# Kernel optimization log

Measured on AMD Instinct MI355X. Metric: run time of the kernel, lower is better.

## Reference

```python
import jax, jax.numpy as jnp
from jax import lax
import numpy as np

DIM = 48
HEADS = 2
HIDDEN = 96  # int(dim * 2.0)
EPS_LN = 1e-5
EPS_NORM = 1e-12


def _ln(x, w, b):
    # WithBias LayerNorm over channel dim (dim=1 in NCHW == last dim in b,(hw),c)
    mu = jnp.mean(x, axis=1, keepdims=True)
    var = jnp.var(x, axis=1, keepdims=True)
    return (x - mu) / jnp.sqrt(var + EPS_LN) * w[None, :, None, None] + b[None, :, None, None]


def _conv1x1(x, w, b):
    # w: [O, C, 1, 1]
    return jnp.einsum('bchw,oc->bohw', x, w[:, :, 0, 0]) + b[None, :, None, None]


def _dwconv3(x, w, b):
    # w: [C, 1, 3, 3], groups=C
    y = lax.conv_general_dilated(x, w, (1, 1), 'SAME',
                                 feature_group_count=x.shape[1],
                                 dimension_numbers=('NCHW', 'OIHW', 'NCHW'))
    return y + b[None, :, None, None]


def _l2norm(x):
    n = jnp.sqrt(jnp.sum(x * x, axis=-1, keepdims=True))
    return x / jnp.maximum(n, EPS_NORM)


def setup_inputs() -> dict:
    key = jax.random.key(0)
    ks = jax.random.split(key, 12)
    s = 0.02
    inp = {
        'x': jax.random.normal(ks[0], (2, DIM, 64, 64), jnp.float32),
        'norm1_w': jnp.ones((DIM,), jnp.float32),
        'norm1_b': jnp.zeros((DIM,), jnp.float32),
        'qkv_w': jax.random.normal(ks[1], (DIM * 3, DIM, 1, 1), jnp.float32) * s,
        'qkv_b': jnp.zeros((DIM * 3,), jnp.float32),
        'qkvdw_w': jax.random.normal(ks[2], (DIM * 3, 1, 3, 3), jnp.float32) * s,
        'qkvdw_b': jnp.zeros((DIM * 3,), jnp.float32),
        'temperature': jnp.ones((HEADS, 1, 1), jnp.float32),
        'proj_w': jax.random.normal(ks[3], (DIM, DIM, 1, 1), jnp.float32) * s,
        'proj_b': jnp.zeros((DIM,), jnp.float32),
        'norm2_w': jnp.ones((DIM,), jnp.float32),
        'norm2_b': jnp.zeros((DIM,), jnp.float32),
        'fi_w': jax.random.normal(ks[4], (HIDDEN * 2, DIM, 1, 1), jnp.float32) * s,
        'fi_b': jnp.zeros((HIDDEN * 2,), jnp.float32),
        'fdw_w': jax.random.normal(ks[5], (HIDDEN * 2, 1, 3, 3), jnp.float32) * s,
        'fdw_b': jnp.zeros((HIDDEN * 2,), jnp.float32),
        'fo_w': jax.random.normal(ks[6], (DIM, HIDDEN, 1, 1), jnp.float32) * s,
        'fo_b': jnp.zeros((DIM,), jnp.float32),
    }
    return inp


def _block(x, norm1_w, norm1_b, qkv_w, qkv_b, qkvdw_w, qkvdw_b, temperature,
           proj_w, proj_b, norm2_w, norm2_b, fi_w, fi_b, fdw_w, fdw_b, fo_w, fo_b):
    b, c, h, w = x.shape
    n = h * w
    chead = c // HEADS
    # --- attention branch ---
    xn = _ln(x, norm1_w, norm1_b)
    qkv = _dwconv3(_conv1x1(xn, qkv_w, qkv_b), qkvdw_w, qkvdw_b)
    q, k, v = jnp.split(qkv, 3, axis=1)
    def to_heads(t):  # [b, heads*chead, h, w] -> [b, heads, n, chead]
        return t.reshape(b, HEADS, chead, n).transpose(0, 1, 3, 2)
    q, k, v = to_heads(q), to_heads(k), to_heads(v)
    q = _l2norm(q)
    k = _l2norm(k)
    attn = jnp.einsum('bhnc,bhmc->bhnm', q, k) * temperature[None]
    attn = jax.nn.softmax(attn, axis=-1)
    out = jnp.einsum('bhnm,bhmc->bhnc', attn, v)
    out = out.transpose(0, 1, 3, 2).reshape(b, c, h, w)
    x = x + _conv1x1(out, proj_w, proj_b)
    # --- ffn branch ---
    xn = _ln(x, norm2_w, norm2_b)
    y = _dwconv3(_conv1x1(xn, fi_w, fi_b), fdw_w, fdw_b)
    y1, y2 = jnp.split(y, 2, axis=1)
    y = jax.nn.gelu(y1, approximate=False) * y2
    x = x + _conv1x1(y, fo_w, fo_b)
    return x


def reference(x, norm1_w, norm1_b, qkv_w, qkv_b, qkvdw_w, qkvdw_b, temperature,
              proj_w, proj_b, norm2_w, norm2_b, fi_w, fi_b, fdw_w, fdw_b, fo_w, fo_b):
    return _block(x, norm1_w, norm1_b, qkv_w, qkv_b, qkvdw_w, qkvdw_b, temperature,
                  proj_w, proj_b, norm2_w, norm2_b, fi_w, fi_b, fdw_w, fdw_b, fo_w, fo_b)
```

## Files before the change

### kernel.cpp

```cpp
#include <hip/hip_runtime.h>
#include <hip/hip_bf16.h>
#include <math.h>

#define NPIX 4096
#define NB 2

typedef __attribute__((ext_vector_type(8))) short short8;
typedef __attribute__((ext_vector_type(4))) short short4s;
typedef __attribute__((ext_vector_type(4))) float floatx4;

static __device__ inline short f2bf(float f) {
    union { float f; unsigned u; } v; v.f = f;
    unsigned r = (v.u + 0x7FFFu + ((v.u >> 16) & 1u)) >> 16;
    return (short)r;
}
static __device__ inline float bf2f(short s) {
    union { unsigned u; float f; } v;
    v.u = ((unsigned)(unsigned short)s) << 16;
    return v.f;
}
static __device__ inline unsigned pk2(float a, float b) {
    __hip_bfloat162 pk = __float22bfloat162_rn(make_float2(a, b));
    return *(unsigned*)&pk;
}

__global__ void k_prepw(const float* __restrict__ qkvw, const float* __restrict__ fiw,
                        const float* __restrict__ fow, const float* __restrict__ projw,
                        short* __restrict__ qkvwbf, short* __restrict__ fiwbf,
                        short* __restrict__ fowbf, short* __restrict__ projwbf) {
    int idx = blockIdx.x * 256 + threadIdx.x;
    if (idx < 144 * 64) {
        int o = idx >> 6, c = idx & 63;
        qkvwbf[idx] = (c < 48) ? f2bf(qkvw[o * 48 + c]) : (short)0;
        return;
    }
    idx -= 144 * 64;
    if (idx < 192 * 64) {
        int o = idx >> 6, c = idx & 63;
        fiwbf[idx] = (c < 48) ? f2bf(fiw[o * 48 + c]) : (short)0;
        return;
    }
    idx -= 192 * 64;
    if (idx < 48 * 96) {
        fowbf[idx] = f2bf(fow[idx]);
        return;
    }
    idx -= 48 * 96;
    if (idx < 48 * 64) {
        int o = idx >> 6, c = idx & 63;
        int h = c >> 5, cc = c & 31;
        projwbf[idx] = (cc < 24) ? f2bf(projw[o * 48 + h * 24 + cc]) : (short)0;
    }
}

__global__ __launch_bounds__(256) void k_qkv_fused(
    const float* __restrict__ xin, const float* __restrict__ n1w, const float* __restrict__ n1b,
    const short* __restrict__ qkvwbf, const float* __restrict__ qkvb,
    const float* __restrict__ dww, const float* __restrict__ dwb,
    const float* __restrict__ temp,
    short* __restrict__ Qbf, short* __restrict__ Kbf, short* __restrict__ Vbf)
{
    int px0 = blockIdx.x * 16;
    int y = blockIdx.y, b = blockIdx.z;
    int t = threadIdx.x;
    int w = t >> 6, lane = t & 63, l15 = lane & 15, quad = lane >> 4;

    __shared__ __align__(16) short xn[64][72];
    __shared__ short qkv[64][148];
    __shared__ float q2[16][148];
    __shared__ float red[4][64], redq[4][64];
    __shared__ float muS[64], rsS[64];
    __shared__ float dwwS[1296], dwbS[144];
    __shared__ short vmask[64];

    for (int u = t; u < 1296; u += 256) dwwS[u] = dww[u];
    if (t < 144) dwbS[t] = dwb[t];

    int pp = t & 63, cg = t >> 6;
    int rr = pp / 18, ix = pp - rr * 18;
    int yy = y + rr - 1, xpx = px0 - 1 + ix;
    bool pv = (pp < 54) && ((unsigned)yy < 64u) && ((unsigned)xpx < 64u);
    if (cg == 0) vmask[pp] = pv ? (short)1 : (short)0;

    float v[12]; float s = 0.f, sq = 0.f;
    if (pv) {
        size_t pbase = (size_t)(yy * 64 + xpx);
#pragma unroll
        for (int j = 0; j < 12; j++) {
            float vv = xin[((size_t)b * 48 + cg * 12 + j) * NPIX + pbase];
            v[j] = vv; s += vv; sq += vv * vv;
        }
    } else {
#pragma unroll
        for (int j = 0; j < 12; j++) v[j] = 0.f;
    }
    red[cg][pp] = s; redq[cg][pp] = sq;
    __syncthreads();
    if (t < 64) {
        float ss = red[0][t] + red[1][t] + red[2][t] + red[3][t];
        float qq = redq[0][t] + redq[1][t] + redq[2][t] + redq[3][t];
        float mu = ss * (1.f / 48.f);
        float var = qq * (1.f / 48.f) - mu * mu;
        muS[t] = mu; rsS[t] = rsqrtf(var + 1e-5f);
    }
    __syncthreads();
    {
        float mu = muS[pp], rs = rsS[pp];
#pragma unroll
        for (int j = 0; j < 12; j++) {
            int c = cg * 12 + j;
            xn[pp][c] = f2bf((v[j] - mu) * rs * n1w[c] + n1b[c]);
        }
        short8 z8 = {};
        if (cg == 0) *(short8*)&xn[pp][48] = z8;
        else if (cg == 1) *(short8*)&xn[pp][56] = z8;
    }
    __syncthreads();
    floatx4 zf = {0.f, 0.f, 0.f, 0.f};
    for (int job = w; job < 36; job += 4) {
        int pt = job / 9, ot = job % 9;
        short8 a0 = *(const short8*)&xn[pt * 16 + l15][quad * 8];
        short8 a1 = *(const short8*)&xn[pt * 16 + l15][32 + quad * 8];
        const short* wb = qkvwbf + (ot * 16 + l15) * 64;
        short8 b0 = *(const short8*)(wb + quad * 8);
        short8 b1 = *(const short8*)(wb + 32 + quad * 8);
        floatx4 c = __builtin_amdgcn_mfma_f32_16x16x32_bf16(a0, b0, zf, 0, 0, 0);
        c = __builtin_amdgcn_mfma_f32_16x16x32_bf16(a1, b1, c, 0, 0, 0);
        int oc = ot * 16 + l15;
        float bi = qkvb[oc];
#pragma unroll
        for (int r = 0; r < 4; r++) {
            int opp = pt * 16 + quad * 4 + r;
            qkv[opp][oc] = vmask[opp] ? f2bf(c[r] + bi) : (short)0;
        }
    }
    __syncthreads();
    {
        int i = t & 15, g = t >> 4;
        for (int cc = 0; cc < 9; cc++) {
            int c = g * 9 + cc;
            const float* wp = dwwS + c * 9;
            float acc = dwbS[c];
#pragma unroll
            for (int dy = 0; dy < 3; dy++)
#pragma unroll
                for (int dx = 0; dx < 3; dx++)
                    acc += bf2f(qkv[dy * 18 + i + dx][c]) * wp[dy * 3 + dx];
            q2[i][c] = acc;
        }
    }
    __syncthreads();
    if (t < 128) {
        int i = t & 15, h = (t >> 4) & 1, sel = t >> 5;
        int n = y * 64 + px0 + i;
        int bh = b * 2 + h;
        if (sel < 2) {
            float vv2[24]; float ss = 0.f;
            int base = sel * 48 + h * 24;
#pragma unroll
            for (int c = 0; c < 24; c++) { vv2[c] = q2[i][base + c]; ss += vv2[c] * vv2[c]; }
            float sc = ((sel == 0) ? temp[h] : 1.f) / fmaxf(sqrtf(ss), 1e-12f);
            short qs[32];
#pragma unroll
            for (int c = 0; c < 24; c++) qs[c] = f2bf(vv2[c] * sc);
#pragma unroll
            for (int c = 24; c < 32; c++) qs[c] = 0;
            short* dst = ((sel == 0) ? Qbf : Kbf) + ((size_t)bh * NPIX + n) * 32;
#pragma unroll
            for (int i8 = 0; i8 < 4; i8++) {
                short8 st;
#pragma unroll
                for (int j = 0; j < 8; j++) st[j] = qs[i8 * 8 + j];
                *(short8*)(dst + i8 * 8) = st;
            }
        } else {
            int half = sel - 2;
            int r5 = n & 31;
            int pos = (r5 < 16) ? ((r5 >> 2) * 8 + (r5 & 3))
                                : (((r5 & 15) >> 2) * 8 + (r5 & 3) + 4);
            int vcol = (n & ~31) + pos;
#pragma unroll
            for (int cc = 0; cc < 12; cc++) {
                int c = half * 12 + cc;
                Vbf[((size_t)bh * 32 + c) * NPIX + vcol] = f2bf(q2[i][96 + h * 24 + c]);
            }
            if (half == 1) {
#pragma unroll
                for (int c = 24; c < 32; c++)
                    Vbf[((size_t)bh * 32 + c) * NPIX + vcol] = 0;
            }
        }
    }
}

__global__ __launch_bounds__(1024) void k_attn_mfma2(
    const short* __restrict__ Qbf, const short* __restrict__ Kbf,
    const short* __restrict__ Vbf, short* __restrict__ O)
{
    int qt = blockIdx.x, bh = blockIdx.y;
    int t = threadIdx.x;
    int tg = t & 255, g = t >> 8;
    int wloc = (t >> 6) & 3, lane = t & 63, l15 = lane & 15, quad = lane >> 4;

    __shared__ __align__(16) short tileK[4][2][64][40];
    __shared__ __align__(16) short tileV[4][2][32][72];
    __shared__ float Ocomb[4][64][33];
    __shared__ float Lcomb[4][64];

    int qrow0 = qt * 64 + wloc * 16;
    short8 bq = *(const short8*)(Qbf + ((size_t)bh * NPIX + qrow0 + l15) * 32 + quad * 8);

    int krow = tg >> 2, kseg = tg & 3;
    int vch = tg >> 3, vseg = tg & 7;
    const short* srcK = Kbf + ((size_t)bh * NPIX + krow) * 32 + kseg * 8;
    const short* srcV = Vbf + ((size_t)(bh * 32 + vch)) * NPIX + vseg * 8;

    int key0 = g * 1024;
    *(short8*)&tileK[g][0][krow][kseg * 8] = *(const short8*)(srcK + (size_t)key0 * 32);
    *(short8*)&tileV[g][0][vch][vseg * 8]  = *(const short8*)(srcV + key0);

    floatx4 zf = {0.f, 0.f, 0.f, 0.f};
    floatx4 o0 = zf, o1 = zf;
    float ls = 0.f;

    const int NKT = 16;
    for (int kt = 0; kt < NKT; kt++) {
        __syncthreads();
        int cur = kt & 1;
        short8 ldK = {}, ldV = {};
        if (kt < NKT - 1) {
            int kabs = key0 + (kt + 1) * 64;
            ldK = *(const short8*)(srcK + (size_t)kabs * 32);
            ldV = *(const short8*)(srcV + kabs);
        }
        short8 ka0 = *(const short8*)&tileK[g][cur][l15][quad * 8];
        short8 ka1 = *(const short8*)&tileK[g][cur][16 + l15][quad * 8];
        short8 ka2 = *(const short8*)&tileK[g][cur][32 + l15][quad * 8];
        short8 ka3 = *(const short8*)&tileK[g][cur][48 + l15][quad * 8];
        floatx4 s0 = __builtin_amdgcn_mfma_f32_16x16x32_bf16(ka0, bq, zf, 0, 0, 0);
        floatx4 s1 = __builtin_amdgcn_mfma_f32_16x16x32_bf16(ka1, bq, zf, 0, 0, 0);
        floatx4 s2 = __builtin_amdgcn_mfma_f32_16x16x32_bf16(ka2, bq, zf, 0, 0, 0);
        floatx4 s3 = __builtin_amdgcn_mfma_f32_16x16x32_bf16(ka3, bq, zf, 0, 0, 0);
        float e0[4], e1[4], e2[4], e3[4];
#pragma unroll
        for (int r = 0; r < 4; r++) {
            e0[r] = __expf(s0[r]); e1[r] = __expf(s1[r]);
            e2[r] = __expf(s2[r]); e3[r] = __expf(s3[r]);
            ls += (e0[r] + e1[r]) + (e2[r] + e3[r]);
        }
        short8 p01, p23;
        {
            unsigned* u01 = (unsigned*)&p01;
            unsigned* u23 = (unsigned*)&p23;
            u01[0] = pk2(e0[0], e0[1]); u01[1] = pk2(e0[2], e0[3]);
            u01[2] = pk2(e1[0], e1[1]); u01[3] = pk2(e1[2], e1[3]);
            u23[0] = pk2(e2[0], e2[1]); u23[1] = pk2(e2[2], e2[3]);
            u23[2] = pk2(e3[0], e3[1]); u23[3] = pk2(e3[2], e3[3]);
        }
        short8 va00 = *(const short8*)&tileV[g][cur][l15][quad * 8];
        short8 va01 = *(const short8*)&tileV[g][cur][l15][32 + quad * 8];
        short8 va10 = *(const short8*)&tileV[g][cur][16 + l15][quad * 8];
        short8 va11 = *(const short8*)&tileV[g][cur][16 + l15][32 + quad * 8];
        o0 = __builtin_amdgcn_mfma_f32_16x16x32_bf16(va00, p01, o0, 0, 0, 0);
        o0 = __builtin_amdgcn_mfma_f32_16x16x32_bf16(va01, p23, o0, 0, 0, 0);
        o1 = __builtin_amdgcn_mfma_f32_16x16x32_bf16(va10, p01, o1, 0, 0, 0);
        o1 = __builtin_amdgcn_mfma_f32_16x16x32_bf16(va11, p23, o1, 0, 0, 0);
        if (kt < NKT - 1) {
            *(short8*)&tileK[g][1 - cur][krow][kseg * 8] = ldK;
            *(short8*)&tileV[g][1 - cur][vch][vseg * 8]  = ldV;
        }
    }
    ls += __shfl_xor(ls, 16, 64);
    ls += __shfl_xor(ls, 32, 64);
    int qi = wloc * 16 + l15;
#pragma unroll
    for (int r = 0; r < 4; r++) {
        Ocomb[g][qi][quad * 4 + r]      = o0[r];
        Ocomb[g][qi][16 + quad * 4 + r] = o1[r];
    }
    if (quad == 0) Lcomb[g][qi] = ls;
    __syncthreads();
    {
        int qq = t >> 4, cp = t & 15;
        float l4 = Lcomb[0][qq] + Lcomb[1][qq] + Lcomb[2][qq] + Lcomb[3][qq];
        float inv = 1.f / l4;
        float sa = (Ocomb[0][qq][2 * cp] + Ocomb[1][qq][2 * cp] +
                    Ocomb[2][qq][2 * cp] + Ocomb[3][qq][2 * cp]) * inv;
        float sb = (Ocomb[0][qq][2 * cp + 1] + Ocomb[1][qq][2 * cp + 1] +
                    Ocomb[2][qq][2 * cp + 1] + Ocomb[3][qq][2 * cp + 1]) * inv;
        int b = bh >> 1, h = bh & 1;
        int n = qt * 64 + qq;
        *(unsigned*)(O + ((size_t)b * NPIX + n) * 64 + h * 32 + 2 * cp) = pk2(sa, sb);
    }
}

__global__ __launch_bounds__(256) void k_tail_fused(
    const float* __restrict__ xin, const short* __restrict__ O,
    const short* __restrict__ projwbf, const float* __restrict__ projb,
    const float* __restrict__ n2w, const float* __restrict__ n2b,
    const short* __restrict__ fiwbf, const float* __restrict__ fib,
    const float* __restrict__ fdww, const float* __restrict__ fdwb,
    const short* __restrict__ fowbf, const float* __restrict__ fob,
    float* __restrict__ out)
{
    int px0 = blockIdx.x * 16;
    int y = blockIdx.y, b = blockIdx.z;
    int t = threadIdx.x;
    int w = t >> 6, lane = t & 63, l15 = lane & 15, quad = lane >> 4;

    __shared__ float x1s[64][53];
    __shared__ __align__(16) short xn2[64][72];
    __shared__ short ypre[56][196];
    __shared__ __align__(16) short yv[16][104];
    __shared__ float red[4][64], redq[4][64];
    __shared__ float muS[64], rsS[64];
    __shared__ float fdwwS[1728], fdwbS[192];
    __shared__ short vmask[64];
    __shared__ int nidx[64];

    for (int u = t; u < 1728; u += 256) fdwwS[u] = fdww[u];
    if (t < 192) fdwbS[t] = fdwb[t];
    if (t < 64) {
        int rr = t / 18, ix = t - rr * 18;
        int yy = y + rr - 1, xpx = px0 - 1 + ix;
        bool pv = (t < 54) && ((unsigned)yy < 64u) && ((unsigned)xpx < 64u);
        vmask[t] = pv ? (short)1 : (short)0;
        int n = yy * 64 + xpx;
        n = n < 0 ? 0 : (n > 4095 ? 4095 : n);
        nidx[t] = n;
    }
    __syncthreads();

    floatx4 zf = {0.f, 0.f, 0.f, 0.f};
    for (int job = w; job < 12; job += 4) {
        int pt = job / 3, ot = job % 3;
        const short* oa = O + ((size_t)b * NPIX + nidx[pt * 16 + l15]) * 64;
        short8 a0 = *(const short8*)(oa + quad * 8);
        short8 a1 = *(const short8*)(oa + 32 + quad * 8);
        const short* wb = projwbf + (ot * 16 + l15) * 64;
        short8 b0 = *(const short8*)(wb + quad * 8);
        short8 b1 = *(const short8*)(wb + 32 + quad * 8);
        floatx4 c = __builtin_amdgcn_mfma_f32_16x16x32_bf16(a0, b0, zf, 0, 0, 0);
        c = __builtin_amdgcn_mfma_f32_16x16x32_bf16(a1, b1, c, 0, 0, 0);
        int oc = ot * 16 + l15;
        float bi = projb[oc];
#pragma unroll
        for (int r = 0; r < 4; r++) {
            int opp = pt * 16 + quad * 4 + r;
            x1s[opp][oc] = xin[((size_t)b * 48 + oc) * NPIX + nidx[opp]] + c[r] + bi;
        }
    }
    __syncthreads();
    int pp = t & 63, cg = t >> 6;
    {
        float v[12]; float s = 0.f, sq = 0.f;
#pragma unroll
        for (int j = 0; j < 12; j++) {
            float vv = x1s[pp][cg * 12 + j];
            v[j] = vv; s += vv; sq += vv * vv;
        }
        red[cg][pp] = s; redq[cg][pp] = sq;
        __syncthreads();
        if (t < 64) {
            float ss = red[0][t] + red[1][t] + red[2][t] + red[3][t];
            float qq = redq[0][t] + redq[1][t] + redq[2][t] + redq[3][t];
            float mu = ss * (1.f / 48.f);
            float var = qq * (1.f / 48.f) - mu * mu;
            muS[t] = mu; rsS[t] = rsqrtf(var + 1e-5f);
        }
        __syncthreads();
        float mu = muS[pp], rs = rsS[pp];
#pragma unroll
        for (int j = 0; j < 12; j++) {
            int c = cg * 12 + j;
            xn2[pp][c] = f2bf((v[j] - mu) * rs * n2w[c] + n2b[c]);
        }
        short8 z8 = {};
        if (cg == 0) *(short8*)&xn2[pp][48] = z8;
        else if (cg == 1) *(short8*)&xn2[pp][56] = z8;
    }
    __syncthreads();
    for (int job = w; job < 48; job += 4) {
        int pt = job / 12, ot = job % 12;
        short8 a0 = *(const short8*)&xn2[pt * 16 + l15][quad * 8];
        short8 a1 = *(const short8*)&xn2[pt * 16 + l15][32 + quad * 8];
        const short* wb = fiwbf + (ot * 16 + l15) * 64;
        short8 b0 = *(const short8*)(wb + quad * 8);
        short8 b1 = *(const short8*)(wb + 32 + quad * 8);
        floatx4 c = __builtin_amdgcn_mfma_f32_16x16x32_bf16(a0, b0, zf, 0, 0, 0);
        c = __builtin_amdgcn_mfma_f32_16x16x32_bf16(a1, b1, c, 0, 0, 0);
        int oc = ot * 16 + l15;
        float bi = fib[oc];
#pragma unroll
        for (int r = 0; r < 4; r++) {
            int opp = pt * 16 + quad * 4 + r;
            if (opp < 56) ypre[opp][oc] = vmask[opp] ? f2bf(c[r] + bi) : (short)0;
        }
    }
    __syncthreads();
    {
        int i = t & 15, gg = t >> 4;
        for (int cc = 0; cc < 6; cc++) {
            int c = gg * 6 + cc;
            const float* wp  = fdwwS + c * 9;
            const float* wp2 = fdwwS + (c + 96) * 9;
            float a = fdwbS[c], g2v = fdwbS[c + 96];
#pragma unroll
            for (int dy = 0; dy < 3; dy++)
#pragma unroll
                for (int dx = 0; dx < 3; dx++) {
                    int ppi = dy * 18 + i + dx;
                    a   += bf2f(ypre[ppi][c])      * wp[dy * 3 + dx];
                    g2v += bf2f(ypre[ppi][c + 96]) * wp2[dy * 3 + dx];
                }
            float ge = 0.5f * a * (1.f + erff(a * 0.70710678118654752f));
            yv[i][c] = f2bf(ge * g2v);
        }
        short8 z8 = {};
        if (gg == 0) *(short8*)&yv[i][96] = z8;
    }
    __syncthreads();
    if (w < 3) {
        floatx4 c = zf;
#pragma unroll
        for (int k = 0; k < 3; k++) {
            short8 a  = *(const short8*)&yv[l15][k * 32 + quad * 8];
            short8 bb = *(const short8*)(fowbf + (w * 16 + l15) * 96 + k * 32 + quad * 8);
            c = __builtin_amdgcn_mfma_f32_16x16x32_bf16(a, bb, c, 0, 0, 0);
        }
        int oc = w * 16 + l15;
        float bi = fob[oc];
#pragma unroll
        for (int r = 0; r < 4; r++) {
            int i = quad * 4 + r;
            size_t idx = ((size_t)b * 48 + oc) * NPIX + y * 64 + px0 + i;
            out[idx] = x1s[19 + i][oc] + c[r] + bi;
        }
    }
}

extern "C" void kernel_launch(void* const* d_in, const int* in_sizes, int n_in,
                              void* d_out, int out_size, void* d_ws, size_t ws_size,
                              hipStream_t stream) {
    const float* x       = (const float*)d_in[0];
    const float* n1w     = (const float*)d_in[1];
    const float* n1b     = (const float*)d_in[2];
    const float* qkv_w   = (const float*)d_in[3];
    const float* qkv_b   = (const float*)d_in[4];
    const float* qkvdw_w = (const float*)d_in[5];
    const float* qkvdw_b = (const float*)d_in[6];
    const float* temp    = (const float*)d_in[7];
    const float* proj_w  = (const float*)d_in[8];
    const float* proj_b  = (const float*)d_in[9];
    const float* n2w     = (const float*)d_in[10];
    const float* n2b     = (const float*)d_in[11];
    const float* fi_w    = (const float*)d_in[12];
    const float* fi_b    = (const float*)d_in[13];
    const float* fdw_w   = (const float*)d_in[14];
    const float* fdw_b   = (const float*)d_in[15];
    const float* fo_w    = (const float*)d_in[16];
    const float* fo_b    = (const float*)d_in[17];

    short* sws = (short*)d_ws;
    short* Qbf     = sws;
    short* Kbf     = Qbf + 524288;
    short* Vbf     = Kbf + 524288;
    short* Obuf    = Vbf + 524288;
    short* qkvwbf  = Obuf + 524288;
    short* fiwbf   = qkvwbf + 9216;
    short* fowbf   = fiwbf + 12288;
    short* projwbf = fowbf + 4608;

    {
        int total = 144 * 64 + 192 * 64 + 48 * 96 + 48 * 64;
        k_prepw<<<(total + 255) / 256, 256, 0, stream>>>(qkv_w, fi_w, fo_w, proj_w,
                                                         qkvwbf, fiwbf, fowbf, projwbf);
    }
    {
        dim3 g(4, 64, NB);
        k_qkv_fused<<<g, 256, 0, stream>>>(x, n1w, n1b, qkvwbf, qkv_b,
                                           qkvdw_w, qkvdw_b, temp, Qbf, Kbf, Vbf);
    }
    {
        dim3 g(64, 4);
        k_attn_mfma2<<<g, 1024, 0, stream>>>(Qbf, Kbf, Vbf, Obuf);
    }
    {
        dim3 g(4, 64, NB);
        k_tail_fused<<<g, 256, 0, stream>>>(x, Obuf, projwbf, proj_b, n2w, n2b,
                                            fiwbf, fi_b, fdw_w, fdw_b, fowbf, fo_b,
                                            (float*)d_out);
    }
}
```

Baseline: 139.5 us.

## Fold weight bf16 conversion into qkv kernel and switch softmax to exp2

```diff
diff --git a/kernel.cpp b/kernel.cpp
--- a/kernel.cpp
+++ b/kernel.cpp
@@ -6,7 +6,6 @@
 #define NB 2
 
 typedef __attribute__((ext_vector_type(8))) short short8;
-typedef __attribute__((ext_vector_type(4))) short short4s;
 typedef __attribute__((ext_vector_type(4))) float floatx4;
 
 static __device__ inline short f2bf(float f) {
@@ -24,41 +23,15 @@
     return *(unsigned*)&pk;
 }
 
-__global__ void k_prepw(const float* __restrict__ qkvw, const float* __restrict__ fiw,
-                        const float* __restrict__ fow, const float* __restrict__ projw,
-                        short* __restrict__ qkvwbf, short* __restrict__ fiwbf,
-                        short* __restrict__ fowbf, short* __restrict__ projwbf) {
-    int idx = blockIdx.x * 256 + threadIdx.x;
-    if (idx < 144 * 64) {
-        int o = idx >> 6, c = idx & 63;
-        qkvwbf[idx] = (c < 48) ? f2bf(qkvw[o * 48 + c]) : (short)0;
-        return;
-    }
-    idx -= 144 * 64;
-    if (idx < 192 * 64) {
-        int o = idx >> 6, c = idx & 63;
-        fiwbf[idx] = (c < 48) ? f2bf(fiw[o * 48 + c]) : (short)0;
-        return;
-    }
-    idx -= 192 * 64;
-    if (idx < 48 * 96) {
-        fowbf[idx] = f2bf(fow[idx]);
-        return;
-    }
-    idx -= 48 * 96;
-    if (idx < 48 * 64) {
-        int o = idx >> 6, c = idx & 63;
-        int h = c >> 5, cc = c & 31;
-        projwbf[idx] = (cc < 24) ? f2bf(projw[o * 48 + h * 24 + cc]) : (short)0;
-    }
-}
-
 __global__ __launch_bounds__(256) void k_qkv_fused(
     const float* __restrict__ xin, const float* __restrict__ n1w, const float* __restrict__ n1b,
-    const short* __restrict__ qkvwbf, const float* __restrict__ qkvb,
+    const float* __restrict__ qkvw, const float* __restrict__ qkvb,
     const float* __restrict__ dww, const float* __restrict__ dwb,
     const float* __restrict__ temp,
-    short* __restrict__ Qbf, short* __restrict__ Kbf, short* __restrict__ Vbf)
+    const float* __restrict__ fiw, const float* __restrict__ fow,
+    const float* __restrict__ projw,
+    short* __restrict__ Qbf, short* __restrict__ Kbf, short* __restrict__ Vbf,
+    short* __restrict__ fiwbf, short* __restrict__ fowbf, short* __restrict__ projwbf)
 {
     int px0 = blockIdx.x * 16;
     int y = blockIdx.y, b = blockIdx.z;
@@ -67,34 +40,54 @@
 
     __shared__ __align__(16) short xn[64][72];
     __shared__ short qkv[64][148];
-    __shared__ float q2[16][148];
+    __shared__ union {
+        short wA[144][72];
+        struct { float q2[16][148]; float dwwS[1296]; float dwbS[144]; } d;
+    } u;
     __shared__ float red[4][64], redq[4][64];
     __shared__ float muS[64], rsS[64];
-    __shared__ float dwwS[1296], dwbS[144];
     __shared__ short vmask[64];
 
-    for (int u = t; u < 1296; u += 256) dwwS[u] = dww[u];
-    if (t < 144) dwbS[t] = dwb[t];
-
-    int pp = t & 63, cg = t >> 6;
+    {
+        int bid = (blockIdx.z * 64 + blockIdx.y) * 4 + blockIdx.x;
+        int gt = bid * 256 + t;
+        if (gt < 12288) {
+            int o = gt >> 6, c = gt & 63;
+            fiwbf[gt] = (c < 48) ? f2bf(fiw[o * 48 + c]) : (short)0;
+        } else if (gt < 16896) {
+            int u2 = gt - 12288;
+            fowbf[u2] = f2bf(fow[u2]);
+        } else if (gt < 19968) {
+            int u2 = gt - 16896;
+            int o = u2 >> 6, c = u2 & 63;
+            int h = c >> 5, cc = c & 31;
+            projwbf[u2] = (cc < 24) ? f2bf(projw[o * 48 + h * 24 + cc]) : (short)0;
+        }
+    }
+    for (int u2 = t; u2 < 144 * 64; u2 += 256) {
+        int o = u2 >> 6, c = u2 & 63;
+        u.wA[o][c] = (c < 48) ? f2bf(qkvw[o * 48 + c]) : (short)0;
+    }
+
+    int pp = t & 63, cg2 = t >> 6;
     int rr = pp / 18, ix = pp - rr * 18;
     int yy = y + rr - 1, xpx = px0 - 1 + ix;
     bool pv = (pp < 54) && ((unsigned)yy < 64u) && ((unsigned)xpx < 64u);
-    if (cg == 0) vmask[pp] = pv ? (short)1 : (short)0;
+    if (cg2 == 0) vmask[pp] = pv ? (short)1 : (short)0;
 
     float v[12]; float s = 0.f, sq = 0.f;
     if (pv) {
         size_t pbase = (size_t)(yy * 64 + xpx);
 #pragma unroll
-        for (int j = 0; j < 12; j++) {
-            float vv = xin[((size_t)b * 48 + cg * 12 + j) * NPIX + pbase];
-            v[j] = vv; s += vv; sq += vv * vv;
+        for (int j2 = 0; j2 < 12; j2++) {
+            float vv = xin[((size_t)b * 48 + cg2 * 12 + j2) * NPIX + pbase];
+            v[j2] = vv; s += vv; sq += vv * vv;
         }
     } else {
 #pragma unroll
-        for (int j = 0; j < 12; j++) v[j] = 0.f;
-    }
-    red[cg][pp] = s; redq[cg][pp] = sq;
+        for (int j2 = 0; j2 < 12; j2++) v[j2] = 0.f;
+    }
+    red[cg2][pp] = s; redq[cg2][pp] = sq;
     __syncthreads();
     if (t < 64) {
         float ss = red[0][t] + red[1][t] + red[2][t] + red[3][t];
@@ -107,13 +100,13 @@
     {
         float mu = muS[pp], rs = rsS[pp];
 #pragma unroll
-        for (int j = 0; j < 12; j++) {
-            int c = cg * 12 + j;
-            xn[pp][c] = f2bf((v[j] - mu) * rs * n1w[c] + n1b[c]);
+        for (int j2 = 0; j2 < 12; j2++) {
+            int c = cg2 * 12 + j2;
+            xn[pp][c] = f2bf((v[j2] - mu) * rs * n1w[c] + n1b[c]);
         }
         short8 z8 = {};
-        if (cg == 0) *(short8*)&xn[pp][48] = z8;
-        else if (cg == 1) *(short8*)&xn[pp][56] = z8;
+        if (cg2 == 0) *(short8*)&xn[pp][48] = z8;
+        else if (cg2 == 1) *(short8*)&xn[pp][56] = z8;
     }
     __syncthreads();
     floatx4 zf = {0.f, 0.f, 0.f, 0.f};
@@ -121,7 +114,7 @@
         int pt = job / 9, ot = job % 9;
         short8 a0 = *(const short8*)&xn[pt * 16 + l15][quad * 8];
         short8 a1 = *(const short8*)&xn[pt * 16 + l15][32 + quad * 8];
-        const short* wb = qkvwbf + (ot * 16 + l15) * 64;
+        const short* wb = &u.wA[ot * 16 + l15][0];
         short8 b0 = *(const short8*)(wb + quad * 8);
         short8 b1 = *(const short8*)(wb + 32 + quad * 8);
         floatx4 c = __builtin_amdgcn_mfma_f32_16x16x32_bf16(a0, b0, zf, 0, 0, 0);
@@ -135,18 +128,21 @@
         }
     }
     __syncthreads();
-    {
-        int i = t & 15, g = t >> 4;
+    for (int u2 = t; u2 < 1296; u2 += 256) u.d.dwwS[u2] = dww[u2];
+    if (t < 144) u.d.dwbS[t] = dwb[t];
+    __syncthreads();
+    {
+        int i = t & 15, g3 = t >> 4;
         for (int cc = 0; cc < 9; cc++) {
-            int c = g * 9 + cc;
-            const float* wp = dwwS + c * 9;
-            float acc = dwbS[c];
+            int c = g3 * 9 + cc;
+            const float* wp = u.d.dwwS + c * 9;
+            float acc = u.d.dwbS[c];
 #pragma unroll
             for (int dy = 0; dy < 3; dy++)
 #pragma unroll
                 for (int dx = 0; dx < 3; dx++)
                     acc += bf2f(qkv[dy * 18 + i + dx][c]) * wp[dy * 3 + dx];
-            q2[i][c] = acc;
+            u.d.q2[i][c] = acc;
         }
     }
     __syncthreads();
@@ -158,8 +154,8 @@
             float vv2[24]; float ss = 0.f;
             int base = sel * 48 + h * 24;
 #pragma unroll
-            for (int c = 0; c < 24; c++) { vv2[c] = q2[i][base + c]; ss += vv2[c] * vv2[c]; }
-            float sc = ((sel == 0) ? temp[h] : 1.f) / fmaxf(sqrtf(ss), 1e-12f);
+            for (int c = 0; c < 24; c++) { vv2[c] = u.d.q2[i][base + c]; ss += vv2[c] * vv2[c]; }
+            float sc = ((sel == 0) ? temp[h] * 1.44269504089f : 1.f) / fmaxf(sqrtf(ss), 1e-12f);
             short qs[32];
 #pragma unroll
             for (int c = 0; c < 24; c++) qs[c] = f2bf(vv2[c] * sc);
@@ -170,7 +166,7 @@
             for (int i8 = 0; i8 < 4; i8++) {
                 short8 st;
 #pragma unroll
-                for (int j = 0; j < 8; j++) st[j] = qs[i8 * 8 + j];
+                for (int j2 = 0; j2 < 8; j2++) st[j2] = qs[i8 * 8 + j2];
                 *(short8*)(dst + i8 * 8) = st;
             }
         } else {
@@ -182,7 +178,7 @@
 #pragma unroll
             for (int cc = 0; cc < 12; cc++) {
                 int c = half * 12 + cc;
-                Vbf[((size_t)bh * 32 + c) * NPIX + vcol] = f2bf(q2[i][96 + h * 24 + c]);
+                Vbf[((size_t)bh * 32 + c) * NPIX + vcol] = f2bf(u.d.q2[i][96 + h * 24 + c]);
             }
             if (half == 1) {
 #pragma unroll
@@ -244,8 +240,8 @@
         float e0[4], e1[4], e2[4], e3[4];
 #pragma unroll
         for (int r = 0; r < 4; r++) {
-            e0[r] = __expf(s0[r]); e1[r] = __expf(s1[r]);
-            e2[r] = __expf(s2[r]); e3[r] = __expf(s3[r]);
+            e0[r] = exp2f(s0[r]); e1[r] = exp2f(s1[r]);
+            e2[r] = exp2f(s2[r]); e3[r] = exp2f(s3[r]);
             ls += (e0[r] + e1[r]) + (e2[r] + e3[r]);
         }
         short8 p01, p23;
@@ -351,15 +347,15 @@
         }
     }
     __syncthreads();
-    int pp = t & 63, cg = t >> 6;
+    int pp = t & 63, cg2 = t >> 6;
     {
         float v[12]; float s = 0.f, sq = 0.f;
 #pragma unroll
-        for (int j = 0; j < 12; j++) {
-            float vv = x1s[pp][cg * 12 + j];
-            v[j] = vv; s += vv; sq += vv * vv;
-        }
-        red[cg][pp] = s; redq[cg][pp] = sq;
+        for (int j2 = 0; j2 < 12; j2++) {
+            float vv = x1s[pp][cg2 * 12 + j2];
+            v[j2] = vv; s += vv; sq += vv * vv;
+        }
+        red[cg2][pp] = s; redq[cg2][pp] = sq;
         __syncthreads();
         if (t < 64) {
             float ss = red[0][t] + red[1][t] + red[2][t] + red[3][t];
@@ -371,13 +367,13 @@
         __syncthreads();
         float mu = muS[pp], rs = rsS[pp];
 #pragma unroll
-        for (int j = 0; j < 12; j++) {
-            int c = cg * 12 + j;
-            xn2[pp][c] = f2bf((v[j] - mu) * rs * n2w[c] + n2b[c]);
+        for (int j2 = 0; j2 < 12; j2++) {
+            int c = cg2 * 12 + j2;
+            xn2[pp][c] = f2bf((v[j2] - mu) * rs * n2w[c] + n2b[c]);
         }
         short8 z8 = {};
-        if (cg == 0) *(short8*)&xn2[pp][48] = z8;
-        else if (cg == 1) *(short8*)&xn2[pp][56] = z8;
+        if (cg2 == 0) *(short8*)&xn2[pp][48] = z8;
+        else if (cg2 == 1) *(short8*)&xn2[pp][56] = z8;
     }
     __syncthreads();
     for (int job = w; job < 48; job += 4) {
@@ -466,20 +462,16 @@
     short* Kbf     = Qbf + 524288;
     short* Vbf     = Kbf + 524288;
     short* Obuf    = Vbf + 524288;
-    short* qkvwbf  = Obuf + 524288;
-    short* fiwbf   = qkvwbf + 9216;
+    short* fiwbf   = Obuf + 524288;
     short* fowbf   = fiwbf + 12288;
     short* projwbf = fowbf + 4608;
 
     {
-        int total = 144 * 64 + 192 * 64 + 48 * 96 + 48 * 64;
-        k_prepw<<<(total + 255) / 256, 256, 0, stream>>>(qkv_w, fi_w, fo_w, proj_w,
-                                                         qkvwbf, fiwbf, fowbf, projwbf);
-    }
-    {
         dim3 g(4, 64, NB);
-        k_qkv_fused<<<g, 256, 0, stream>>>(x, n1w, n1b, qkvwbf, qkv_b,
-                                           qkvdw_w, qkvdw_b, temp, Qbf, Kbf, Vbf);
+        k_qkv_fused<<<g, 256, 0, stream>>>(x, n1w, n1b, qkv_w, qkv_b,
+                                           qkvdw_w, qkvdw_b, temp,
+                                           fi_w, fo_w, proj_w,
+                                           Qbf, Kbf, Vbf, fiwbf, fowbf, projwbf);
     }
     {
         dim3 g(64, 4);
```

New measurement: 153.6 us. 1.1x slower.
